# Performance work log

Measured on AMD Instinct MI355X. Metric: run time of the kernel, lower is better.

## Reference

```python
import jax, jax.numpy as jnp
import numpy as np
from functools import lru_cache

B_IN, B_L1, B_L2 = 112, 28, 14


def _wigner_ds(l, betas):
    """Wigner-d matrices d^l_{m'm}(beta) (quantum norm, centered order, CS phase)
    via d(beta) = expm(beta*K), K = -(J+ - J-)/2 real antisymmetric; iK is
    Hermitian so we eigendecompose once and phase-rotate for all betas."""
    if l == 0:
        return np.ones((len(betas), 1, 1))
    m = np.arange(-l, l)
    c = np.sqrt(l * (l + 1) - m * (m + 1))  # ladder coefficients m -> m+1
    K = np.zeros((2 * l + 1, 2 * l + 1))
    i = np.arange(2 * l)
    K[i + 1, i] = -0.5 * c
    K[i, i + 1] = 0.5 * c
    lam, V = np.linalg.eigh(1j * K)
    ph = np.exp(-1j * np.outer(betas, lam))  # [n_beta, 2l+1]
    return np.einsum('ak,bk,ck->bac', V, ph, V.conj()).real  # [n_beta, m', m]


def _quad_weights(b):
    """Kostelec-Rockmore SOFT quadrature weights on the 2b beta grid."""
    j = np.arange(2 * b)
    k = np.arange(b)
    s = (np.sin(np.pi * (2 * j[:, None] + 1) * (2 * k[None, :] + 1) / (4. * b))
         / (2 * k[None, :] + 1)).sum(1)
    w = (2. / b) * np.sin(np.pi * (2 * j + 1) / (4. * b)) * s
    return (w * 2. * np.pi / (2 * b) ** 2).astype(np.float32)


@lru_cache(maxsize=None)
def _s2_wigner(b, nl):
    """Weighted forward-S2-FFT table: n=0 column of d^l, [2b, nl^2]."""
    betas = (np.arange(2 * b) + 0.5) / (2 * b) * np.pi
    w = _quad_weights(b)
    cols = [_wigner_ds(l, betas)[:, :, l] * w[:, None] for l in range(nl)]
    return np.concatenate(cols, 1).astype(np.float32)


@lru_cache(maxsize=None)
def _so3_wigner(b, nl, weighted):
    """SO3 transform table: [2b, sum_l (2l+1)^2]; quadrature-weighted for the
    forward transform, (2l+1)-scaled for the inverse."""
    betas = (np.arange(2 * b) + 0.5) / (2 * b) * np.pi
    w = _quad_weights(b)
    cols = []
    for l in range(nl):
        d = _wigner_ds(l, betas)
        d = d * (w[:, None, None] if weighted else float(2 * l + 1))
        cols.append(d.reshape(2 * b, -1))
    return np.concatenate(cols, 1).astype(np.float32)


def _freq_idx(l, n):
    # centered frequencies m=-l..l mapped to FFT bin order of an n-point FFT
    return np.concatenate([np.arange(n - l, n), np.arange(l + 1)]) if l > 0 else np.arange(1)


def s2_fft(x, b_in, b_out):
    # x: complex [z, 2b, 2b] over (beta, alpha) -> spectral [b_out^2, z]
    wig = _s2_wigner(b_in, b_out)
    xf = jnp.fft.fft(x, axis=2)  # FFT over alpha, unnormalized
    outs = []
    for l in range(b_out):
        w = jnp.asarray(wig[:, l * l:l * l + 2 * l + 1]).astype(x.dtype)
        xx = xf[:, :, _freq_idx(l, 2 * b_in)]
        outs.append(jnp.einsum('bm,zbm->mz', w, xx))
    return jnp.concatenate(outs, 0)


def so3_fft(x, b_in, b_out):
    # x: complex [z, 2b, 2b, 2b] over (beta, alpha, gamma) -> [nspec, z]
    wig = _so3_wigner(b_in, b_out, True)
    xf = jnp.fft.fftn(x, axes=(2, 3))
    outs, begin = [], 0
    for l in range(b_out):
        L = 2 * l + 1
        idx = _freq_idx(l, 2 * b_in)
        xx = xf[:, :, idx[:, None], idx[None, :]]
        w = jnp.asarray(wig[:, begin:begin + L * L].reshape(2 * b_in, L, L)).astype(x.dtype)
        outs.append(jnp.einsum('bmn,zbmn->mnz', w, xx).reshape(L * L, -1))
        begin += L * L
    return jnp.concatenate(outs, 0)


def so3_rifft(spec, b):
    # spec: complex [sum_{l<b}(2l+1)^2, z] -> real [z, 2b, 2b, 2b]
    wig = _so3_wigner(b, b, False)
    z = spec.shape[1]
    F = jnp.zeros((z, 2 * b, 2 * b, 2 * b), spec.dtype)
    begin = 0
    for l in range(b):
        L = 2 * l + 1
        sl = spec[begin:begin + L * L].reshape(L, L, z)
        w = jnp.asarray(wig[:, begin:begin + L * L].reshape(2 * b, L, L)).astype(spec.dtype)
        t = jnp.einsum('mnz,bmn->zbmn', sl, w)
        idx = _freq_idx(l, 2 * b)
        F = F.at[:, :, idx[:, None], idx[None, :]].add(t)
        begin += L * L
    # unnormalized inverse FFT over (alpha, gamma), matching torch.ifft * (2b)^2
    return (jnp.fft.ifftn(F, axes=(2, 3)) * (2 * b) ** 2).real


def s2_conv(x, w, bias, b_in, b_out):
    B, Cin = x.shape[0], x.shape[1]
    Cout = w.shape[2]
    xs = s2_fft(x.reshape(B * Cin, 2 * b_in, 2 * b_in).astype(jnp.complex64), b_in, b_out)
    xs = xs.reshape(-1, B, Cin)  # [l*m, B, Cin]
    y = jax.lax.complex(w[..., 0], w[..., 1])  # [l*m, Cin, Cout]
    outs = []
    for l in range(b_out):  # s2_mm: z_l[m,n] = sum_i x_l[m,i] conj(y_l[n,i])
        s = slice(l * l, l * l + 2 * l + 1)
        Fz = jnp.einsum('mzi,nio->mnzo', xs[s], jnp.conj(y[s]))
        outs.append(Fz.reshape(-1, B, Cout))
    zs = jnp.concatenate(outs, 0).reshape(-1, B * Cout)
    out = so3_rifft(zs, b_out).reshape(B, Cout, 2 * b_out, 2 * b_out, 2 * b_out)
    return out + bias


def so3_conv(x, w, bias, b_in, b_out):
    B, Cin = x.shape[0], x.shape[1]
    Cout = w.shape[2]
    xs = so3_fft(x.reshape(B * Cin, 2 * b_in, 2 * b_in, 2 * b_in).astype(jnp.complex64), b_in, b_out)
    xs = xs.reshape(-1, B, Cin)  # [l*m*n, B, Cin]
    y = jax.lax.complex(w[..., 0], w[..., 1])  # [l*m*n, Cin, Cout]
    outs, begin = [], 0
    for l in range(b_out):  # so3_mm: z_l[m,n] = sum_{k,i} conj(x_l[m,k,i]) y_l[n,k,i]
        L = 2 * l + 1
        X = xs[begin:begin + L * L].reshape(L, L, B, Cin)
        Y = y[begin:begin + L * L].reshape(L, L, Cin, Cout)
        Fz = jnp.einsum('mkzi,nkio->mnzo', jnp.conj(X), Y)
        outs.append(Fz.reshape(L * L, B, Cout))
        begin += L * L
    zs = jnp.concatenate(outs, 0).reshape(-1, B * Cout)
    out = so3_rifft(zs, b_out).reshape(B, Cout, 2 * b_out, 2 * b_out, 2 * b_out)
    return out + bias


def so3_integrate(x):
    # x: [B, C, beta, alpha, gamma]; sum over alpha,gamma + quadrature over beta
    b = x.shape[-1] // 2
    w = jnp.asarray(_quad_weights(b))
    return jnp.einsum('zcbag,b->zc', x, w)


def _nspec_so3(b):
    return b * (4 * b * b - 1) // 3


def setup_inputs() -> dict:
    key = jax.random.key(0)
    ks = jax.random.split(key, 8)
    B = 4
    sc = 1e-3  # keep activations in a sane range through 5 spectral convs
    return {
        'x': jax.random.normal(ks[0], (B, 3, 2 * B_IN, 2 * B_IN), jnp.float32),
        'w1': jax.random.normal(ks[1], (B_L1 ** 2, 3, 32, 2), jnp.float32) * sc,
        'b1': jnp.zeros((1, 32, 1, 1, 1), jnp.float32),
        'w2': jax.random.normal(ks[2], (_nspec_so3(B_L2), 32, 64, 2), jnp.float32) * sc,
        'b2': jnp.zeros((1, 64, 1, 1, 1), jnp.float32),
        'w3': jax.random.normal(ks[3], (_nspec_so3(B_L2), 64, 128, 2), jnp.float32) * sc,
        'b3': jnp.zeros((1, 128, 1, 1, 1), jnp.float32),
        'w4': jax.random.normal(ks[4], (_nspec_so3(B_L2), 128, 64, 2), jnp.float32) * sc,
        'b4': jnp.zeros((1, 64, 1, 1, 1), jnp.float32),
        'w5': jax.random.normal(ks[5], (_nspec_so3(B_L2), 64, 40, 2), jnp.float32) * sc,
        'b5': jnp.zeros((1, 40, 1, 1, 1), jnp.float32),
        'w_out': jax.random.normal(ks[6], (10, 40), jnp.float32) * 0.1,
        'b_out': jnp.zeros((10,), jnp.float32),
    }


def reference(x, w1, b1, w2, b2, w3, b3, w4, b4, w5, b5, w_out, b_out):
    h = jax.nn.relu(s2_conv(x, w1, b1, B_IN, B_L1))
    h = jax.nn.relu(so3_conv(h, w2, b2, B_L1, B_L2))
    h = jax.nn.relu(so3_conv(h, w3, b3, B_L2, B_L2))
    h = jax.nn.relu(so3_conv(h, w4, b4, B_L2, B_L2))
    h = jax.nn.relu(so3_conv(h, w5, b5, B_L2, B_L2))
    h = so3_integrate(h)
    return h @ w_out.T + b_out
```

## Files before the change

### kernel.cpp

```cpp
#include <hip/hip_runtime.h>
#include <cmath>
#include <cstring>
#include <vector>



__global__ void kg_idx(int4* __restrict__ LMN28, int4* __restrict__ LMN14,
                       int* __restrict__ IDX1) {
  int l = blockIdx.x;
  int L = 2*l + 1, ofs = l*(4*l*l - 1)/3;
  for (int i = threadIdx.x; i < L*L; i += blockDim.x) {
    int a = i / L, c = i - a*L;
    int4 v = make_int4(l, a - l, c - l, 0);
    LMN28[ofs + i] = v;
    if (l < 14) LMN14[ofs + i] = v;
  }
  for (int a = threadIdx.x; a < L; a += blockDim.x)
    IDX1[l*l + a] = (a - l) + 27;
}

__global__ void kg_tw(float2* __restrict__ E224, float2* __restrict__ EF56,
                      float2* __restrict__ EI56, float2* __restrict__ EF28,
                      float2* __restrict__ EI28) {
  int t = blockIdx.x*256 + threadIdx.x;
  const float TP = 6.283185307179586f;
  if (t < 12320) {
    int mi = t/224, a = t - mi*224;
    int r = ((mi - 27)*a) % 224;
    float ang = -TP*r/224.f;
    E224[t] = make_float2(cosf(ang), sinf(ang)); return;
  }
  t -= 12320;
  if (t < 1512) {
    int ki = t/56, g = t - ki*56;
    int r = ((ki - 13)*g) % 56;
    float ang = -TP*r/56.f;
    EF56[t] = make_float2(cosf(ang), sinf(ang)); return;
  }
  t -= 1512;
  if (t < 3080) {
    int a = t/55, mi = t - a*55;
    int r = ((mi - 27)*a) % 56;
    float ang = TP*r/56.f;
    EI56[t] = make_float2(cosf(ang), sinf(ang)); return;
  }
  t -= 3080;
  if (t < 756) {
    int ki = t/28, g = t - ki*28;
    int r = ((ki - 13)*g) % 28;
    float ang = -TP*r/28.f;
    EF28[t] = make_float2(cosf(ang), sinf(ang)); return;
  }
  t -= 756;
  if (t < 756) {
    int a = t/27, mi = t - a*27;
    int r = ((mi - 13)*a) % 28;
    float ang = TP*r/28.f;
// ... 228 lines not shown
  }
}

template<int NA, int NF>
__global__ __launch_bounds__(256)
void kf2_dfta(const float2* __restrict__ XA, const float2* __restrict__ EF,
              float2* __restrict__ Xf, int rowsC) {
  int ki = blockIdx.x;
  int mt = blockIdx.y;
  int row = blockIdx.z*256 + threadIdx.x;
  if (row >= rowsC) return;
  float2 acc[14];
  #pragma unroll
  for (int u = 0; u < 14; ++u) acc[u] = make_float2(0.f, 0.f);
  const float2* xp = XA + (size_t)ki*rowsC + row;
  for (int a = 0; a < NA; ++a) {
    float2 v = xp[(size_t)a*NF*rowsC];
    #pragma unroll
    for (int u = 0; u < 14; ++u) {
      int mi = mt*14 + u; if (mi >= NF) mi = NF-1;
      float2 e = EF[mi*NA + a];
      acc[u].x += v.x*e.x - v.y*e.y;
      acc[u].y += v.x*e.y + v.y*e.x;
    }
  }
  #pragma unroll
  for (int u = 0; u < 14; ++u) {
    int mi = mt*14 + u;
    if (mi < NF) Xf[((size_t)mi*NF + ki)*rowsC + row] = acc[u];
  }
}

__global__ void k8_wigfwd(const float2* __restrict__ XfT,
                          const float* __restrict__ WT,
                          const int4* __restrict__ LMN,
                          float2* __restrict__ XS,
                          int NB, int ZC, int z0, int Ztot) {
  int spec = blockIdx.x;
  int zl = threadIdx.x;
  int4 t = LMN[spec];
  int mi = t.y + 13, ni = t.z + 13;
  float2 acc = make_float2(0.f, 0.f);
  size_t base = (size_t)(mi*27 + ni) * ((size_t)NB*ZC);
  for (int b = 0; b < NB; ++b) {
    float w = WT[(size_t)spec*NB + b];
    float2 v = XfT[base + (size_t)b*ZC + zl];
    acc.x += w*v.x; acc.y += w*v.y;
  }
  XS[(size_t)spec*Ztot + z0 + zl] = acc;
}

template<int CI, int CO>
__global__ __launch_bounds__(256)
void k9_gemm3(const float2* __restrict__ XS, const float2* __restrict__ W,
              const int4* __restrict__ tasks, float2* __restrict__ ZSo) {
  constexpr int Zin = 4*CI, Zout = 4*CO;
  constexpr int LOG2CI = (CI==32) ? 5 : (CI==64) ? 6 : 7;
  int4 tk = tasks[blockIdx.x];
  int l = tk.x, m0 = tk.y, c0 = tk.z;
  int L = 2*l + 1;
  int ofs = l*(4*l*l - 1)/3;
  int N = L*CO, K = L*CI;
  __shared__ float2 As[16][33];
  __shared__ float2 Bs[16][64];
  int t = threadIdx.x;
  int ob = t & 63, kb0 = t >> 6;
  int c = c0 + ob;
  bool colOK = c < N;
  int n = colOK ? c / CO : 0;
  int o = c - n*CO;
  size_t bbase = ((size_t)(ofs + n*L))*(size_t)(CI*CO) + o;
  int q = t >> 6, j = t & 63;
  float2 acc[8];
  #pragma unroll
  for (int u = 0; u < 8; ++u) acc[u] = make_float2(0.f, 0.f);

  for (int k0 = 0; k0 < K; k0 += 16) {
    #pragma unroll
    for (int h = 0; h < 2; ++h) {
      int fi = t + h*256;
      int row = fi >> 4, tc = fi & 15;
      int m = m0 + (row >> 2), zb = row & 3;
      int kk = k0 + tc;
      float2 av = make_float2(0.f, 0.f);
      if (m < L) {
        int kq = kk >> LOG2CI, ii = kk & (CI-1);
        float2 xv = XS[((size_t)(ofs + m*L + kq))*Zin + (size_t)zb*CI + ii];
        av = make_float2(xv.x, -xv.y);
      }
      As[tc][row] = av;
    }
    #pragma unroll
    for (int j2 = 0; j2 < 4; ++j2) {
      int kb = kb0*4 + j2;
      float2 wv = make_float2(0.f, 0.f);
      if (colOK) wv = W[bbase + (size_t)(k0 + kb)*CO];
      Bs[kb][ob] = wv;
    }
    __syncthreads();
    for (int kk2 = 0; kk2 < 16; ++kk2) {
      float2 b = Bs[kk2][j];
      #pragma unroll
      for (int u = 0; u < 8; ++u) {
        float2 a = As[kk2][u*4 + q];
        acc[u].x += a.x*b.x - a.y*b.y;
        acc[u].y += a.x*b.y + a.y*b.x;
      }
    }
    __syncthreads();
  }
  if (colOK) {
    #pragma unroll
    for (int u = 0; u < 8; ++u) {
      int m = m0 + u;
      if (m < L) {
        ZSo[((size_t)(ofs + m*L + n))*Zout + (size_t)q*CO + o] = acc[u];
      }
    }
  }
}

__global__ void k10a_colsum(const float* __restrict__ Ht, float* __restrict__ Cp,
                            int rows, int cols, int rowsPer) {
  int col = blockIdx.x*256 + threadIdx.x;
  if (col >= cols) return;
  int r0 = blockIdx.y*rowsPer;
  int r1 = r0 + rowsPer; if (r1 > rows) r1 = rows;
  float acc = 0.f;
  for (int r = r0; r < r1; ++r) acc += Ht[(size_t)r*cols + col];
  Cp[(size_t)blockIdx.y*cols + col] = acc;
}

__global__ void k10a_fin(const float* __restrict__ Cp, const float* __restrict__ QW,
                         float* __restrict__ S, int Zt, int NB, int nparts) {
  int z = blockIdx.x*64 + threadIdx.x;
  if (z >= Zt) return;
  int cols = NB*Zt;
  float acc = 0.f;
  for (int b = 0; b < NB; ++b) {
    float cs = 0.f;
    for (int p = 0; p < nparts; ++p) cs += Cp[(size_t)p*cols + b*Zt + z];
    acc += cs * QW[b];
  }
  S[z] = acc;
}

__global__ void k10b_fc(const float* __restrict__ S,
                        const float* __restrict__ Wout,
                        const float* __restrict__ bout,
                        float* __restrict__ out) {
  int t = threadIdx.x;
  if (t < 40) {
    int zb = t / 10, c = t % 10;
    float acc = bout[c];
    for (int o = 0; o < 40; ++o) acc += S[zb*40 + o] * Wout[c*40 + o];
    out[zb*10 + c] = acc;
  }
}


static const size_t U_VT    = 0;
static const size_t U_LAM   = 117040;
static const size_t U_QW224 = U_LAM + 3136;
static const size_t U_QW56  = U_QW224 + 896;
static const size_t U_QW28  = U_QW56 + 224;
static const size_t U_TK2   = U_QW28 + 112;
static const size_t U_TK3   = U_TK2 + 24576;
static const size_t U_TK4   = U_TK3 + 24576;
static const size_t U_TK5   = U_TK4 + 24576;
static const size_t U_BYTES = U_TK5 + 24576;

struct WsOff {
  size_t up, ws2t, wi28t, wf28t, wi14t, wf14t, e224, ef56, ei56, ef28, ei28,
         lmn28, lmn14, idx1, zs1, xsf, zso, HA, HB, S, fixedEnd;
};

static WsOff wsOff() {
  WsOff o; size_t c = 0;
  auto take = [&](size_t bytes) { size_t r = c; c = (c + bytes + 255) & ~(size_t)255; return r; };
  o.up    = take(U_BYTES);
  o.ws2t  = take((size_t)784*224*4);
  o.wi28t = take((size_t)29260*56*4);
  o.wf28t = take((size_t)3654*56*4);
  o.wi14t = take((size_t)3654*28*4);
  o.wf14t = take((size_t)3654*28*4);
  o.e224  = take((size_t)55*224*8);
  o.ef56  = take((size_t)27*56*8);
  o.ei56  = take((size_t)56*55*8);
  o.ef28  = take((size_t)27*28*8);
  o.ei28  = take((size_t)28*27*8);
  o.lmn28 = take((size_t)29260*16);
  o.lmn14 = take((size_t)3654*16);
  o.idx1  = take(784*4);
  o.zs1   = take((size_t)29260*128*8);
  o.xsf   = take((size_t)3654*512*8);
  o.zso   = take((size_t)3654*512*8);
  o.HA    = take((size_t)128*56*56*56*4);
  o.HB    = take((size_t)512*28*28*28*4);
  o.S     = take(16*4480*4 + 1024);
  o.fixedEnd = c;
  return o;
}

static void jacobi_sym(int n, double* A, double* V, double* lam) {
  for (int i = 0; i < n*n; ++i) V[i] = 0.0;
  for (int i = 0; i < n; ++i) V[i*n + i] = 1.0;
  for (int sweep = 0; sweep < 100; ++sweep) {
    double off = 0.0;
    for (int p = 0; p < n; ++p)
      for (int q = p+1; q < n; ++q) off += A[p*n+q]*A[p*n+q];
    if (off < 1e-22) break;
    for (int p = 0; p < n-1; ++p) {
      for (int q = p+1; q < n; ++q) {
        double apq = A[p*n+q];
        if (fabs(apq) < 1e-300) continue;
        double theta = (A[q*n+q] - A[p*n+p]) / (2.0*apq);
        double tt = (theta >= 0 ? 1.0 : -1.0) / (fabs(theta) + sqrt(theta*theta + 1.0));
        double cc = 1.0/sqrt(tt*tt + 1.0), ss = tt*cc;
        for (int i = 0; i < n; ++i) {
          double aip = A[i*n+p], aiq = A[i*n+q];
          A[i*n+p] = cc*aip - ss*aiq;
          A[i*n+q] = ss*aip + cc*aiq;
        }
        for (int i = 0; i < n; ++i) {
          double api = A[p*n+i], aqi = A[q*n+i];
          A[p*n+i] = cc*api - ss*aqi;
          A[q*n+i] = ss*api + cc*aqi;
        }
        for (int i = 0; i < n; ++i) {
          double vip = V[i*n+p], viq = V[i*n+q];
          V[i*n+p] = cc*vip - ss*viq;
          V[i*n+q] = ss*vip + cc*viq;
        }
      }
    }
  }
  for (int i = 0; i < n; ++i) lam[i] = A[i*n+i];
}

extern "C" void kernel_launch(void* const* d_in, const int* in_sizes, int n_in,
                              void* d_out, int out_size, void* d_ws, size_t ws_size,
                              hipStream_t stream) {
  (void)in_sizes; (void)n_in; (void)out_size;
  const WsOff off = wsOff();
  const size_t MINAB = (size_t)3080*32*56*8;
  if (ws_size < off.fixedEnd + 2*MINAB) return;

  const float*  x    = (const float*)d_in[0];
  const float2* w1   = (const float2*)d_in[1];
  const float*  b1   = (const float*)d_in[2];
  const float2* w2   = (const float2*)d_in[3];
  const float*  b2   = (const float*)d_in[4];
  const float2* w3   = (const float2*)d_in[5];
  const float*  b3   = (const float*)d_in[6];
  const float2* w4   = (const float2*)d_in[7];
  const float*  b4   = (const float*)d_in[8];
  const float2* w5   = (const float2*)d_in[9];
  const float*  b5   = (const float*)d_in[10];
  const float*  wout = (const float*)d_in[11];
  const float*  bout = (const float*)d_in[12];
  float* outp = (float*)d_out;
  char* ws = (char*)d_ws;

  char* hb = new char[U_BYTES];
  memset(hb, 0, U_BYTES);
  float* hVT  = (float*)(hb + U_VT);
  float* hLAM = (float*)(hb + U_LAM);
  float* hQW224 = (float*)(hb + U_QW224);
  float* hQW56  = (float*)(hb + U_QW56);
  float* hQW28  = (float*)(hb + U_QW28);
  int4*  hTK[4] = {(int4*)(hb + U_TK2), (int4*)(hb + U_TK3),
                   (int4*)(hb + U_TK4), (int4*)(hb + U_TK5)};

  auto quadw = [](int b, double* w) {
    for (int j = 0; j < 2*b; ++j) {
      double s = 0.0;
      for (int k = 0; k < b; ++k)
        s += sin(M_PI*(2*j+1)*(2*k+1)/(4.0*b)) / (double)(2*k+1);
      w[j] = 2.0/b * sin(M_PI*(2*j+1)/(4.0*b)) * s * 2.0*M_PI/((2.0*b)*(2.0*b));
    }
  };
  std::vector<double> qw224(224), qw56(56), qw28v(28);
  quadw(112, qw224.data()); quadw(28, qw56.data()); quadw(14, qw28v.data());
  for (int j = 0; j < 224; ++j) hQW224[j] = (float)qw224[j];
  for (int j = 0; j < 56;  ++j) hQW56[j]  = (float)qw56[j];
  for (int j = 0; j < 28;  ++j) hQW28[j]  = (float)qw28v[j];

  const int NMAX = 55;
  std::vector<double> T(NMAX*NMAX), V(NMAX*NMAX), lam(NMAX);
  for (int l = 0; l < 28; ++l) {
    int n = 2*l + 1;
    std::fill(T.begin(), T.begin() + n*n, 0.0);
    for (int i = 0; i < n-1; ++i) {
      int m = i - l;
      double c = sqrt((double)(l*(l+1)) - (double)(m*(m+1)));
      T[i*n + i + 1] = 0.5*c;
      T[(i+1)*n + i] = 0.5*c;
    }
    jacobi_sym(n, T.data(), V.data(), lam.data());
    size_t vofs = (size_t)l*(4*l*l - 1)/3;
    for (int i = 0; i < n*n; ++i) hVT[vofs + i] = (float)V[i];
    for (int k = 0; k < n; ++k)  hLAM[l*l + k] = (float)lam[k];
  }

  const int COv[4] = {64, 128, 64, 40};
  int tcnt[4];
  for (int li = 0; li < 4; ++li) {
    int cnt = 0;
    for (int l = 13; l >= 0; --l) {
      int L = 2*l + 1, N = L*COv[li];
      for (int c0 = 0; c0 < N; c0 += 64)
        for (int m0 = 0; m0 < L; m0 += 8)
          hTK[li][cnt++] = make_int4(l, m0, c0, 0);
    }
    tcnt[li] = cnt;
  }

  const float*  dWS2T  = (const float*)(ws + off.ws2t);
  const float*  dWI28T = (const float*)(ws + off.wi28t);
  const float*  dWF28T = (const float*)(ws + off.wf28t);
  const float*  dWI14T = (const float*)(ws + off.wi14t);
  const float*  dWF14T = (const float*)(ws + off.wf14t);
  const float2* dE224  = (const float2*)(ws + off.e224);
  const float2* dEF56  = (const float2*)(ws + off.ef56);
  const float2* dEI56  = (const float2*)(ws + off.ei56);
  const float2* dEF28  = (const float2*)(ws + off.ef28);
  const float2* dEI28  = (const float2*)(ws + off.ei28);
  const int4*   dLMN28 = (const int4*)(ws + off.lmn28);
  const int4*   dLMN14 = (const int4*)(ws + off.lmn14);
  const int*    dIDX1  = (const int*)(ws + off.idx1);
  const float*  dUVT   = (const float*)(ws + off.up + U_VT);
  const float*  dULAM  = (const float*)(ws + off.up + U_LAM);
  const float*  dUQW224= (const float*)(ws + off.up + U_QW224);
  const float*  dUQW56 = (const float*)(ws + off.up + U_QW56);
  const float*  dUQW28 = (const float*)(ws + off.up + U_QW28);
  const int4*   dTK2   = (const int4*)(ws + off.up + U_TK2);
  const int4*   dTK3   = (const int4*)(ws + off.up + U_TK3);
  const int4*   dTK4   = (const int4*)(ws + off.up + U_TK4);
  const int4*   dTK5   = (const int4*)(ws + off.up + U_TK5);
  float2* dZS1 = (float2*)(ws + off.zs1);
  float2* dXSF = (float2*)(ws + off.xsf);
  float2* dZSO = (float2*)(ws + off.zso);
  float*  dHA  = (float*)(ws + off.HA);
  float*  dHB  = (float*)(ws + off.HB);
  float*  dCp  = (float*)(ws + off.S);
  float*  dS   = (float*)(ws + off.S + 16*4480*4);

  size_t ab = ((ws_size - off.fixedEnd)/2) & ~(size_t)255;
  char* Abuf = ws + off.fixedEnd;
  char* Bbuf = Abuf + ab;
  float2* dA = (float2*)Abuf;
  float2* dB = (float2*)Bbuf;
  float2* dXF1 = (float2*)Abuf;
  float2* dXS1 = (float2*)(Abuf + 1182720);

  hipMemcpyAsync(ws + off.up, hb, U_BYTES, hipMemcpyHostToDevice, stream);
  kg_idx<<<28, 256, 0, stream>>>((int4*)(ws + off.lmn28), (int4*)(ws + off.lmn14),
                                 (int*)(ws + off.idx1));
  kg_tw<<<72, 256, 0, stream>>>((float2*)(ws + off.e224), (float2*)(ws + off.ef56),
                                (float2*)(ws + off.ei56), (float2*)(ws + off.ef28),
                                (float2*)(ws + off.ei28));
  kg_wig<<<784, 224, 0, stream>>>(dUVT, dULAM, dUQW224, nullptr,
                                  (float*)(ws + off.ws2t), 224, 0);
  kg_wig<<<29260, 64, 0, stream>>>(dUVT, dULAM, nullptr, dLMN28,
                                   (float*)(ws + off.wi28t), 56, 1);
  kg_wig<<<3654, 64, 0, stream>>>(dUVT, dULAM, dUQW56, dLMN14,
                                  (float*)(ws + off.wf28t), 56, 2);
  kg_wig<<<3654, 64, 0, stream>>>(dUVT, dULAM, nullptr, dLMN14,
                                  (float*)(ws + off.wi14t), 28, 1);
  kg_wig<<<3654, 64, 0, stream>>>(dUVT, dULAM, dUQW28, dLMN14,
                                  (float*)(ws + off.wf14t), 28, 2);

  auto pickPow2 = [&](int Zt, size_t perz)->int {
    int zc = Zt;
    while (zc > 32 && perz*(size_t)zc > ab) zc >>= 1;
    return zc;
  };
  int zc1  = pickPow2(128, (size_t)3080*56*8);
  int zcF2 = pickPow2(128, (size_t)56*27*56*8);
  int zcI  = pickPow2(256, (size_t)756*28*8);
  int zcF  = pickPow2(256, (size_t)28*27*28*8);

  k1_dft_alpha<<<12*224, 64, 0, stream>>>(x, dE224, dXF1);
  k2_s2wig<<<784, 64, 0, stream>>>(dXF1, dWS2T, dIDX1, dXS1);
  k3_combine1<<<29260, 128, 0, stream>>>(dXS1, w1, dLMN28, dZS1);
  for (int z0 = 0; z0 < 128; z0 += zc1) {
    int rowsC = zc1*56;
    k4_wiginv<56,28><<<dim3(3025, zc1/32), 256, 0, stream>>>(dZS1, dWI28T, dA, 128, z0, zc1);
    k5a_idft<55,56><<<dim3(55, 7, (rowsC+255)/256), 256, 0, stream>>>(dA, dEI56, dB, rowsC);
    k5b_idft<55,56><<<dim3(56, (rowsC+63)/64), 256, 0, stream>>>(dB, dEI56, b1, dHA,
                                                                 zc1, z0, 128, 56, 32, rowsC);
  }

  for (int z0 = 0; z0 < 128; z0 += zcF2) {
    int rowsC = zcF2*56;
    kf1_dftg<56,27><<<dim3(56, 2, (rowsC+255)/256), 256, 0, stream>>>(dHA, dEF56, dA,
                                                                      56, 128, z0, zcF2, rowsC);
    kf2_dfta<56,27><<<dim3(27, 2, (rowsC+255)/256), 256, 0, stream>>>(dA, dEF56, dB, rowsC);
    k8_wigfwd<<<3654, zcF2, 0, stream>>>(dB, dWF28T, dLMN14, dXSF, 56, zcF2, z0, 128);
  }
  k9_gemm3<32,64><<<tcnt[0], 256, 0, stream>>>(dXSF, w2, dTK2, dZSO);
  for (int z0 = 0; z0 < 256; z0 += zcI) {
    int rowsC = zcI*28;
    k4_wiginv<28,14><<<dim3(729, zcI/32), 256, 0, stream>>>(dZSO, dWI14T, dA, 256, z0, zcI);
    k5a_idft<27,28><<<dim3(27, 4, (rowsC+255)/256), 256, 0, stream>>>(dA, dEI28, dB, rowsC);
    k5b_idft<27,28><<<dim3(28, (rowsC+63)/64), 256, 0, stream>>>(dB, dEI28, b2, dHB,
                                                                 zcI, z0, 256, 28, 64, rowsC);
  }

  for (int z0 = 0; z0 < 256; z0 += zcF) {
    int rowsC = zcF*28;
    kf1_dftg<28,27><<<dim3(28, 2, (rowsC+255)/256), 256, 0, stream>>>(dHB, dEF28, dA,
                                                                      28, 256, z0, zcF, rowsC);
    kf2_dfta<28,27><<<dim3(27, 2, (rowsC+255)/256), 256, 0, stream>>>(dA, dEF28, dB, rowsC);
    k8_wigfwd<<<3654, zcF, 0, stream>>>(dB, dWF14T, dLMN14, dXSF, 28, zcF, z0, 256);
  }
  k9_gemm3<64,128><<<tcnt[1], 256, 0, stream>>>(dXSF, w3, dTK3, dZSO);
  for (int z0 = 0; z0 < 512; z0 += zcI) {
    int rowsC = zcI*28;
    k4_wiginv<28,14><<<dim3(729, zcI/32), 256, 0, stream>>>(dZSO, dWI14T, dA, 512, z0, zcI);
    k5a_idft<27,28><<<dim3(27, 4, (rowsC+255)/256), 256, 0, stream>>>(dA, dEI28, dB, rowsC);
    k5b_idft<27,28><<<dim3(28, (rowsC+63)/64), 256, 0, stream>>>(dB, dEI28, b3, dHA,
                                                                 zcI, z0, 512, 28, 128, rowsC);
  }

  for (int z0 = 0; z0 < 512; z0 += zcF) {
    int rowsC = zcF*28;
    kf1_dftg<28,27><<<dim3(28, 2, (rowsC+255)/256), 256, 0, stream>>>(dHA, dEF28, dA,
                                                                      28, 512, z0, zcF, rowsC);
    kf2_dfta<28,27><<<dim3(27, 2, (rowsC+255)/256), 256, 0, stream>>>(dA, dEF28, dB, rowsC);
    k8_wigfwd<<<3654, zcF, 0, stream>>>(dB, dWF14T, dLMN14, dXSF, 28, zcF, z0, 512);
  }
  k9_gemm3<128,64><<<tcnt[2], 256, 0, stream>>>(dXSF, w4, dTK4, dZSO);
  for (int z0 = 0; z0 < 256; z0 += zcI) {
    int rowsC = zcI*28;
    k4_wiginv<28,14><<<dim3(729, zcI/32), 256, 0, stream>>>(dZSO, dWI14T, dA, 256, z0, zcI);
    k5a_idft<27,28><<<dim3(27, 4, (rowsC+255)/256), 256, 0, stream>>>(dA, dEI28, dB, rowsC);
    k5b_idft<27,28><<<dim3(28, (rowsC+63)/64), 256, 0, stream>>>(dB, dEI28, b4, dHB,
                                                                 zcI, z0, 256, 28, 64, rowsC);
  }

  for (int z0 = 0; z0 < 256; z0 += zcF) {
    int rowsC = zcF*28;
    kf1_dftg<28,27><<<dim3(28, 2, (rowsC+255)/256), 256, 0, stream>>>(dHB, dEF28, dA,
                                                                      28, 256, z0, zcF, rowsC);
    kf2_dfta<28,27><<<dim3(27, 2, (rowsC+255)/256), 256, 0, stream>>>(dA, dEF28, dB, rowsC);
    k8_wigfwd<<<3654, zcF, 0, stream>>>(dB, dWF14T, dLMN14, dXSF, 28, zcF, z0, 256);
  }
  k9_gemm3<64,40><<<tcnt[3], 256, 0, stream>>>(dXSF, w5, dTK5, dZSO);
  {
    int rowsC = 160*28;
    k4_wiginv<28,14><<<dim3(729, 5), 256, 0, stream>>>(dZSO, dWI14T, dA, 160, 0, 160);
    k5a_idft<27,28><<<dim3(27, 4, (rowsC+255)/256), 256, 0, stream>>>(dA, dEI28, dB, rowsC);
    k5b_idft<27,28><<<dim3(28, (rowsC+63)/64), 256, 0, stream>>>(dB, dEI28, b5, dHA,
                                                                 160, 0, 160, 28, 40, rowsC);
  }

  k10a_colsum<<<dim3(18, 16), 256, 0, stream>>>(dHA, dCp, 784, 4480, 49);
  k10a_fin<<<3, 64, 0, stream>>>(dCp, dUQW28, dS, 160, 28, 16);
  k10b_fc<<<1, 64, 0, stream>>>(dS, wout, bout, outp);
}
```

Measured before the change: 4.336 ms.

## Retile spectral GEMM so each block covers all m rows with register prefetch

The per-degree complex GEMM is reorganised so each block owns 32 output columns (n,o) and the full 4L set of (m,z) rows, instead of 8 m-rows by 64 columns. This means each weight element is read from global memory once rather than once per m-tile. Next-step weight and input tiles are loaded into registers while the current tile is computed from shared memory. The cost is 14 accumulators per thread with predicated work that is wasted for small l, and fewer blocks in flight.

```diff
diff --git a/kernel.cpp b/kernel.cpp
--- a/kernel.cpp
+++ b/kernel.cpp
@@ -337,69 +337,104 @@
 
 template<int CI, int CO>
 __global__ __launch_bounds__(256)
-void k9_gemm3(const float2* __restrict__ XS, const float2* __restrict__ W,
-              const int4* __restrict__ tasks, float2* __restrict__ ZSo) {
+void k9_gemm5(const float2* __restrict__ XS, const float2* __restrict__ W,
+              const int2* __restrict__ tasks, float2* __restrict__ ZSo) {
   constexpr int Zin = 4*CI, Zout = 4*CO;
   constexpr int LOG2CI = (CI==32) ? 5 : (CI==64) ? 6 : 7;
-  int4 tk = tasks[blockIdx.x];
-  int l = tk.x, m0 = tk.y, c0 = tk.z;
+  int2 tk = tasks[blockIdx.x];
+  int l = tk.x, no0 = tk.y;
   int L = 2*l + 1;
   int ofs = l*(4*l*l - 1)/3;
+  int C = 4*L;
   int N = L*CO, K = L*CI;
-  __shared__ float2 As[16][33];
-  __shared__ float2 Bs[16][64];
+  __shared__ float2 Ws[16][32];
+  __shared__ float2 Xs[16][129];
   int t = threadIdx.x;
-  int ob = t & 63, kb0 = t >> 6;
-  int c = c0 + ob;
-  bool colOK = c < N;
-  int n = colOK ? c / CO : 0;
-  int o = c - n*CO;
-  size_t bbase = ((size_t)(ofs + n*L))*(size_t)(CI*CO) + o;
-  int q = t >> 6, j = t & 63;
-  float2 acc[8];
-  #pragma unroll
-  for (int u = 0; u < 8; ++u) acc[u] = make_float2(0.f, 0.f);
-
-  for (int k0 = 0; k0 < K; k0 += 16) {
-    #pragma unroll
-    for (int h = 0; h < 2; ++h) {
-      int fi = t + h*256;
-      int row = fi >> 4, tc = fi & 15;
-      int m = m0 + (row >> 2), zb = row & 3;
-      int kk = k0 + tc;
-      float2 av = make_float2(0.f, 0.f);
-      if (m < L) {
-        int kq = kk >> LOG2CI, ii = kk & (CI-1);
-        float2 xv = XS[((size_t)(ofs + m*L + kq))*Zin + (size_t)zb*CI + ii];
-        av = make_float2(xv.x, -xv.y);
+  int row = t & 31, cg = t >> 5;
+  int nrow = no0 + row;
+  bool rowOK = nrow < N;
+  int n = rowOK ? nrow / CO : 0;
+  int o = nrow - n*CO;
+  size_t wbase = ((size_t)(ofs + n*L))*(size_t)(CI*CO) + o;
+
+  float2 acc[14];
+  #pragma unroll
+  for (int u = 0; u < 14; ++u) acc[u] = make_float2(0.f, 0.f);
+  float2 wreg[2];
+  float2 xreg[7];
+  int nsteps = K >> 4;
+
+  #pragma unroll
+  for (int h = 0; h < 2; ++h) {
+    int kk = cg + h*8;
+    wreg[h] = rowOK ? W[wbase + (size_t)kk*CO] : make_float2(0.f, 0.f);
+  }
+  #pragma unroll
+  for (int h = 0; h < 7; ++h) {
+    int f = t + h*256;
+    int kk = f & 15, col = f >> 4;
+    float2 v = make_float2(0.f, 0.f);
+    if (col < C) {
+      int kq = kk >> LOG2CI, ii = kk & (CI-1);
+      int m = col >> 2, zb = col & 3;
+      float2 xv = XS[((size_t)(ofs + m*L + kq))*Zin + (size_t)zb*CI + ii];
+      v = make_float2(xv.x, -xv.y);
+    }
+    xreg[h] = v;
+  }
+
+  for (int ks = 0; ks < nsteps; ++ks) {
+    __syncthreads();
+    #pragma unroll
+    for (int h = 0; h < 2; ++h) Ws[cg + h*8][row] = wreg[h];
+    #pragma unroll
+    for (int h = 0; h < 7; ++h) {
+      int f = t + h*256;
+      if ((f >> 4) < 128) Xs[f & 15][f >> 4] = xreg[h];
+    }
+    __syncthreads();
+    if (ks + 1 < nsteps) {
+      int k0 = (ks + 1)*16;
+      #pragma unroll
+      for (int h = 0; h < 2; ++h) {
+        int kk = k0 + cg + h*8;
+        wreg[h] = rowOK ? W[wbase + (size_t)kk*CO] : make_float2(0.f, 0.f);
       }
-      As[tc][row] = av;
-    }
-    #pragma unroll
-    for (int j2 = 0; j2 < 4; ++j2) {
-      int kb = kb0*4 + j2;
-      float2 wv = make_float2(0.f, 0.f);
-      if (colOK) wv = W[bbase + (size_t)(k0 + kb)*CO];
-      Bs[kb][ob] = wv;
-    }
-    __syncthreads();
-    for (int kk2 = 0; kk2 < 16; ++kk2) {
-      float2 b = Bs[kk2][j];
       #pragma unroll
-      for (int u = 0; u < 8; ++u) {
-        float2 a = As[kk2][u*4 + q];
-        acc[u].x += a.x*b.x - a.y*b.y;
-        acc[u].y += a.x*b.y + a.y*b.x;
+      for (int h = 0; h < 7; ++h) {
+        int f = t + h*256;
+        int kk = k0 + (f & 15), col = f >> 4;
+        float2 v = make_float2(0.f, 0.f);
+        if (col < C) {
+          int kq = kk >> LOG2CI, ii = kk & (CI-1);
+          int m = col >> 2, zb = col & 3;
+          float2 xv = XS[((size_t)(ofs + m*L + kq))*Zin + (size_t)zb*CI + ii];
+          v = make_float2(xv.x, -xv.y);
+        }
+        xreg[h] = v;
       }
     }
-    __syncthreads();
-  }
-  if (colOK) {
-    #pragma unroll
-    for (int u = 0; u < 8; ++u) {
-      int m = m0 + u;
-      if (m < L) {
-        ZSo[((size_t)(ofs + m*L + n))*Zout + (size_t)q*CO + o] = acc[u];
+    #pragma unroll
+    for (int kk = 0; kk < 16; ++kk) {
+      float2 w = Ws[kk][row];
+      #pragma unroll
+      for (int u = 0; u < 14; ++u) {
+        int col = cg + u*8;
+        if (col < C) {
+          float2 xv = Xs[kk][col];
+          acc[u].x += xv.x*w.x - xv.y*w.y;
+          acc[u].y += xv.x*w.y + xv.y*w.x;
+        }
+      }
+    }
+  }
+  if (rowOK) {
+    #pragma unroll
+    for (int u = 0; u < 14; ++u) {
+      int col = cg + u*8;
+      if (col < C) {
+        int m = col >> 2, zb = col & 3;
+        ZSo[((size_t)(ofs + m*L + n))*Zout + (size_t)zb*CO + o] = acc[u];
       }
     }
   }
@@ -554,8 +589,8 @@
   float* hQW224 = (float*)(hb + U_QW224);
   float* hQW56  = (float*)(hb + U_QW56);
   float* hQW28  = (float*)(hb + U_QW28);
-  int4*  hTK[4] = {(int4*)(hb + U_TK2), (int4*)(hb + U_TK3),
-                   (int4*)(hb + U_TK4), (int4*)(hb + U_TK5)};
+  int2*  hTK[4] = {(int2*)(hb + U_TK2), (int2*)(hb + U_TK3),
+                   (int2*)(hb + U_TK4), (int2*)(hb + U_TK5)};
 
   auto quadw = [](int b, double* w) {
     for (int j = 0; j < 2*b; ++j) {
@@ -594,9 +629,8 @@
     int cnt = 0;
     for (int l = 13; l >= 0; --l) {
       int L = 2*l + 1, N = L*COv[li];
-      for (int c0 = 0; c0 < N; c0 += 64)
-        for (int m0 = 0; m0 < L; m0 += 8)
-          hTK[li][cnt++] = make_int4(l, m0, c0, 0);
+      for (int no0 = 0; no0 < N; no0 += 32)
+        hTK[li][cnt++] = make_int2(l, no0);
     }
     tcnt[li] = cnt;
   }
@@ -619,10 +653,10 @@
   const float*  dUQW224= (const float*)(ws + off.up + U_QW224);
   const float*  dUQW56 = (const float*)(ws + off.up + U_QW56);
   const float*  dUQW28 = (const float*)(ws + off.up + U_QW28);
-  const int4*   dTK2   = (const int4*)(ws + off.up + U_TK2);
-  const int4*   dTK3   = (const int4*)(ws + off.up + U_TK3);
-  const int4*   dTK4   = (const int4*)(ws + off.up + U_TK4);
-  const int4*   dTK5   = (const int4*)(ws + off.up + U_TK5);
+  const int2*   dTK2   = (const int2*)(ws + off.up + U_TK2);
+  const int2*   dTK3   = (const int2*)(ws + off.up + U_TK3);
+  const int2*   dTK4   = (const int2*)(ws + off.up + U_TK4);
+  const int2*   dTK5   = (const int2*)(ws + off.up + U_TK5);
   float2* dZS1 = (float2*)(ws + off.zs1);
   float2* dXSF = (float2*)(ws + off.xsf);
   float2* dZSO = (float2*)(ws + off.zso);
@@ -684,7 +718,7 @@
     kf2_dfta<56,27><<<dim3(27, 2, (rowsC+255)/256), 256, 0, stream>>>(dA, dEF56, dB, rowsC);
     k8_wigfwd<<<3654, zcF2, 0, stream>>>(dB, dWF28T, dLMN14, dXSF, 56, zcF2, z0, 128);
   }
-  k9_gemm3<32,64><<<tcnt[0], 256, 0, stream>>>(dXSF, w2, dTK2, dZSO);
+  k9_gemm5<32,64><<<tcnt[0], 256, 0, stream>>>(dXSF, w2, dTK2, dZSO);
   for (int z0 = 0; z0 < 256; z0 += zcI) {
     int rowsC = zcI*28;
     k4_wiginv<28,14><<<dim3(729, zcI/32), 256, 0, stream>>>(dZSO, dWI14T, dA, 256, z0, zcI);
@@ -700,7 +734,7 @@
     kf2_dfta<28,27><<<dim3(27, 2, (rowsC+255)/256), 256, 0, stream>>>(dA, dEF28, dB, rowsC);
     k8_wigfwd<<<3654, zcF, 0, stream>>>(dB, dWF14T, dLMN14, dXSF, 28, zcF, z0, 256);
   }
-  k9_gemm3<64,128><<<tcnt[1], 256, 0, stream>>>(dXSF, w3, dTK3, dZSO);
+  k9_gemm5<64,128><<<tcnt[1], 256, 0, stream>>>(dXSF, w3, dTK3, dZSO);
   for (int z0 = 0; z0 < 512; z0 += zcI) {
     int rowsC = zcI*28;
     k4_wiginv<28,14><<<dim3(729, zcI/32), 256, 0, stream>>>(dZSO, dWI14T, dA, 512, z0, zcI);
@@ -716,7 +750,7 @@
     kf2_dfta<28,27><<<dim3(27, 2, (rowsC+255)/256), 256, 0, stream>>>(dA, dEF28, dB, rowsC);
     k8_wigfwd<<<3654, zcF, 0, stream>>>(dB, dWF14T, dLMN14, dXSF, 28, zcF, z0, 512);
   }
-  k9_gemm3<128,64><<<tcnt[2], 256, 0, stream>>>(dXSF, w4, dTK4, dZSO);
+  k9_gemm5<128,64><<<tcnt[2], 256, 0, stream>>>(dXSF, w4, dTK4, dZSO);
   for (int z0 = 0; z0 < 256; z0 += zcI) {
     int rowsC = zcI*28;
     k4_wiginv<28,14><<<dim3(729, zcI/32), 256, 0, stream>>>(dZSO, dWI14T, dA, 256, z0, zcI);
@@ -732,7 +766,7 @@
     kf2_dfta<28,27><<<dim3(27, 2, (rowsC+255)/256), 256, 0, stream>>>(dA, dEF28, dB, rowsC);
     k8_wigfwd<<<3654, zcF, 0, stream>>>(dB, dWF14T, dLMN14, dXSF, 28, zcF, z0, 256);
   }
-  k9_gemm3<64,40><<<tcnt[3], 256, 0, stream>>>(dXSF, w5, dTK5, dZSO);
+  k9_gemm5<64,40><<<tcnt[3], 256, 0, stream>>>(dXSF, w5, dTK5, dZSO);
   {
     int rowsC = 160*28;
     k4_wiginv<28,14><<<dim3(729, 5), 256, 0, stream>>>(dZSO, dWI14T, dA, 160, 0, 160);
```

After: 7.859 ms. 81.2% more time.

## Split-K the per-degree spectral GEMM for high l and reduce partials

Applied to the files above, without the earlier changes.

For degrees l>=8, the spectral GEMM's K dimension is split into NS chunks so that more blocks run in parallel on the long, tail-heavy high-l tasks. Partial results from the extra chunks go to a scratch buffer, and a new add kernel folds them into the output. This trades extra global writes, reads and a launch for better load balance and occupancy. It also reuses the B buffer as partial storage and grows the task tables.

```diff
diff --git a/kernel.cpp b/kernel.cpp
--- a/kernel.cpp
+++ b/kernel.cpp
@@ -337,15 +337,23 @@
 
 template<int CI, int CO>
 __global__ __launch_bounds__(256)
-void k9_gemm3(const float2* __restrict__ XS, const float2* __restrict__ W,
-              const int4* __restrict__ tasks, float2* __restrict__ ZSo) {
+void k9_gemm7(const float2* __restrict__ XS, const float2* __restrict__ W,
+              const int4* __restrict__ tasks, float2* __restrict__ ZSo,
+              float2* __restrict__ P, size_t pstride, int NS, int L0) {
   constexpr int Zin = 4*CI, Zout = 4*CO;
   constexpr int LOG2CI = (CI==32) ? 5 : (CI==64) ? 6 : 7;
   int4 tk = tasks[blockIdx.x];
-  int l = tk.x, m0 = tk.y, c0 = tk.z;
+  int l = tk.x, m0 = tk.y, c0 = tk.z, ks = tk.w;
   int L = 2*l + 1;
   int ofs = l*(4*l*l - 1)/3;
   int N = L*CO, K = L*CI;
+  int kb = 0, ke = K;
+  float2* out = ZSo;
+  if (l >= L0) {
+    int chunk = (K/16/NS)*16;
+    kb = ks*chunk; ke = kb + chunk;
+    if (ks > 0) out = P + (size_t)(ks - 1)*pstride;
+  }
   __shared__ float2 As[16][33];
   __shared__ float2 Bs[16][64];
   int t = threadIdx.x;
@@ -360,7 +368,7 @@
   #pragma unroll
   for (int u = 0; u < 8; ++u) acc[u] = make_float2(0.f, 0.f);
 
-  for (int k0 = 0; k0 < K; k0 += 16) {
+  for (int k0 = kb; k0 < ke; k0 += 16) {
     #pragma unroll
     for (int h = 0; h < 2; ++h) {
       int fi = t + h*256;
@@ -377,10 +385,10 @@
     }
     #pragma unroll
     for (int j2 = 0; j2 < 4; ++j2) {
-      int kb = kb0*4 + j2;
+      int kb2 = kb0*4 + j2;
       float2 wv = make_float2(0.f, 0.f);
-      if (colOK) wv = W[bbase + (size_t)(k0 + kb)*CO];
-      Bs[kb][ob] = wv;
+      if (colOK) wv = W[bbase + (size_t)(k0 + kb2)*CO];
+      Bs[kb2][ob] = wv;
     }
     __syncthreads();
     for (int kk2 = 0; kk2 < 16; ++kk2) {
@@ -399,10 +407,22 @@
     for (int u = 0; u < 8; ++u) {
       int m = m0 + u;
       if (m < L) {
-        ZSo[((size_t)(ofs + m*L + n))*Zout + (size_t)q*CO + o] = acc[u];
+        out[((size_t)(ofs + m*L + n))*Zout + (size_t)q*CO + o] = acc[u];
       }
     }
   }
+}
+
+__global__ void kadd(float2* __restrict__ Z, const float2* __restrict__ P,
+                     size_t pstride, size_t offset, size_t count, int nparts) {
+  size_t i = (size_t)blockIdx.x*256 + threadIdx.x;
+  if (i >= count) return;
+  float2 v = Z[offset + i];
+  for (int p = 0; p < nparts; ++p) {
+    float2 w = P[(size_t)p*pstride + offset + i];
+    v.x += w.x; v.y += w.y;
+  }
+  Z[offset + i] = v;
 }
 
 __global__ void k10a_colsum(const float* __restrict__ Ht, float* __restrict__ Cp,
@@ -450,10 +470,10 @@
 static const size_t U_QW56  = U_QW224 + 896;
 static const size_t U_QW28  = U_QW56 + 224;
 static const size_t U_TK2   = U_QW28 + 112;
-static const size_t U_TK3   = U_TK2 + 24576;
-static const size_t U_TK4   = U_TK3 + 24576;
-static const size_t U_TK5   = U_TK4 + 24576;
-static const size_t U_BYTES = U_TK5 + 24576;
+static const size_t U_TK3   = U_TK2 + 32768;
+static const size_t U_TK4   = U_TK3 + 32768;
+static const size_t U_TK5   = U_TK4 + 32768;
+static const size_t U_BYTES = U_TK5 + 32768;
 
 struct WsOff {
   size_t up, ws2t, wi28t, wf28t, wi14t, wf14t, e224, ef56, ei56, ef28, ei28,
@@ -589,14 +609,18 @@
   }
 
   const int COv[4] = {64, 128, 64, 40};
+  const int NSv[4] = {2, 2, 4, 2};
+  const int L0 = 8;
   int tcnt[4];
   for (int li = 0; li < 4; ++li) {
     int cnt = 0;
     for (int l = 13; l >= 0; --l) {
       int L = 2*l + 1, N = L*COv[li];
+      int ns = (l >= L0) ? NSv[li] : 1;
       for (int c0 = 0; c0 < N; c0 += 64)
         for (int m0 = 0; m0 < L; m0 += 8)
-          hTK[li][cnt++] = make_int4(l, m0, c0, 0);
+          for (int ks = 0; ks < ns; ++ks)
+            hTK[li][cnt++] = make_int4(l, m0, c0, ks);
     }
     tcnt[li] = cnt;
   }
@@ -636,6 +660,7 @@
   char* Bbuf = Abuf + ab;
   float2* dA = (float2*)Abuf;
   float2* dB = (float2*)Bbuf;
+  float2* dPart = (float2*)Bbuf;
   float2* dXF1 = (float2*)Abuf;
   float2* dXS1 = (float2*)(Abuf + 1182720);
 
@@ -666,6 +691,14 @@
   int zcI  = pickPow2(256, (size_t)756*28*8);
   int zcF  = pickPow2(256, (size_t)28*27*28*8);
 
+  auto launch_kadd = [&](int Zout, int nparts) {
+    size_t pstride = (size_t)3654*Zout;
+    size_t offs = (size_t)680*Zout;
+    size_t count = (size_t)(3654 - 680)*Zout;
+    kadd<<<(int)((count + 255)/256), 256, 0, stream>>>(dZSO, dPart, pstride,
+                                                       offs, count, nparts);
+  };
+
   k1_dft_alpha<<<12*224, 64, 0, stream>>>(x, dE224, dXF1);
   k2_s2wig<<<784, 64, 0, stream>>>(dXF1, dWS2T, dIDX1, dXS1);
   k3_combine1<<<29260, 128, 0, stream>>>(dXS1, w1, dLMN28, dZS1);
@@ -684,7 +717,9 @@
     kf2_dfta<56,27><<<dim3(27, 2, (rowsC+255)/256), 256, 0, stream>>>(dA, dEF56, dB, rowsC);
     k8_wigfwd<<<3654, zcF2, 0, stream>>>(dB, dWF28T, dLMN14, dXSF, 56, zcF2, z0, 128);
   }
-  k9_gemm3<32,64><<<tcnt[0], 256, 0, stream>>>(dXSF, w2, dTK2, dZSO);
+  k9_gemm7<32,64><<<tcnt[0], 256, 0, stream>>>(dXSF, w2, dTK2, dZSO,
+                                               dPart, (size_t)3654*256, 2, L0);
+  launch_kadd(256, 1);
   for (int z0 = 0; z0 < 256; z0 += zcI) {
     int rowsC = zcI*28;
     k4_wiginv<28,14><<<dim3(729, zcI/32), 256, 0, stream>>>(dZSO, dWI14T, dA, 256, z0, zcI);
@@ -700,7 +735,9 @@
     kf2_dfta<28,27><<<dim3(27, 2, (rowsC+255)/256), 256, 0, stream>>>(dA, dEF28, dB, rowsC);
     k8_wigfwd<<<3654, zcF, 0, stream>>>(dB, dWF14T, dLMN14, dXSF, 28, zcF, z0, 256);
   }
-  k9_gemm3<64,128><<<tcnt[1], 256, 0, stream>>>(dXSF, w3, dTK3, dZSO);
+  k9_gemm7<64,128><<<tcnt[1], 256, 0, stream>>>(dXSF, w3, dTK3, dZSO,
+                                                dPart, (size_t)3654*512, 2, L0);
+  launch_kadd(512, 1);
   for (int z0 = 0; z0 < 512; z0 += zcI) {
     int rowsC = zcI*28;
     k4_wiginv<28,14><<<dim3(729, zcI/32), 256, 0, stream>>>(dZSO, dWI14T, dA, 512, z0, zcI);
@@ -716,7 +753,9 @@
     kf2_dfta<28,27><<<dim3(27, 2, (rowsC+255)/256), 256, 0, stream>>>(dA, dEF28, dB, rowsC);
     k8_wigfwd<<<3654, zcF, 0, stream>>>(dB, dWF14T, dLMN14, dXSF, 28, zcF, z0, 512);
   }
-  k9_gemm3<128,64><<<tcnt[2], 256, 0, stream>>>(dXSF, w4, dTK4, dZSO);
+  k9_gemm7<128,64><<<tcnt[2], 256, 0, stream>>>(dXSF, w4, dTK4, dZSO,
+                                                dPart, (size_t)3654*256, 4, L0);
+  launch_kadd(256, 3);
   for (int z0 = 0; z0 < 256; z0 += zcI) {
     int rowsC = zcI*28;
     k4_wiginv<28,14><<<dim3(729, zcI/32), 256, 0, stream>>>(dZSO, dWI14T, dA, 256, z0, zcI);
@@ -732,7 +771,9 @@
     kf2_dfta<28,27><<<dim3(27, 2, (rowsC+255)/256), 256, 0, stream>>>(dA, dEF28, dB, rowsC);
     k8_wigfwd<<<3654, zcF, 0, stream>>>(dB, dWF14T, dLMN14, dXSF, 28, zcF, z0, 256);
   }
-  k9_gemm3<64,40><<<tcnt[3], 256, 0, stream>>>(dXSF, w5, dTK5, dZSO);
+  k9_gemm7<64,40><<<tcnt[3], 256, 0, stream>>>(dXSF, w5, dTK5, dZSO,
+                                               dPart, (size_t)3654*160, 2, L0);
+  launch_kadd(160, 1);
   {
     int rowsC = 160*28;
     k4_wiginv<28,14><<<dim3(729, 5), 256, 0, stream>>>(dZSO, dWI14T, dA, 160, 0, 160);
```

Result: slower. 4.631 ms (+6.8%).

## Run SO3 spectral complex GEMMs on bf16 MFMA with split-precision emulation

Applied to the files above, without the earlier changes.

Replaces the scalar FP32 complex GEMM in the SO3 convolution layers with an MFMA 16x16x32 bf16 kernel. Each complex operand is split into hi and lo bf16 parts, and three MFMAs (hh, hl, lh) approximate FP32 accuracy. Complex multiplication is encoded as a real GEMM by interleaving real and imaginary parts, with a sign-flipped B layout. Tasks are repacked into single ints. The goal is higher matrix throughput, at the cost of conversion work, smaller tiles with a sync per 16-complex k-step, and slightly lower precision.

```diff
diff --git a/kernel.cpp b/kernel.cpp
--- a/kernel.cpp
+++ b/kernel.cpp
@@ -3,6 +3,16 @@
 #include <cstring>
 #include <vector>
 
+
+using sv8 = __attribute__((ext_vector_type(8))) short;
+using fv4 = __attribute__((ext_vector_type(4))) float;
+
+__device__ __forceinline__ unsigned short bhi(float v) {
+  return (unsigned short)(__float_as_uint(v) >> 16);
+}
+__device__ __forceinline__ float bf2f(unsigned short h) {
+  return __uint_as_float(((unsigned)h) << 16);
+}
 
 
 __global__ void kg_idx(int4* __restrict__ LMN28, int4* __restrict__ LMN14,
@@ -337,69 +347,86 @@
 
 template<int CI, int CO>
 __global__ __launch_bounds__(256)
-void k9_gemm3(const float2* __restrict__ XS, const float2* __restrict__ W,
-              const int4* __restrict__ tasks, float2* __restrict__ ZSo) {
+void k9_mfma(const float2* __restrict__ XS, const float2* __restrict__ W,
+             const int* __restrict__ tasks, float* __restrict__ ZSo) {
   constexpr int Zin = 4*CI, Zout = 4*CO;
   constexpr int LOG2CI = (CI==32) ? 5 : (CI==64) ? 6 : 7;
-  int4 tk = tasks[blockIdx.x];
-  int l = tk.x, m0 = tk.y, c0 = tk.z;
+  int pk = tasks[blockIdx.x];
+  int l  = pk & 15;
+  int m0 = ((pk >> 4) & 15)*16;
+  int c0 = (pk >> 8)*64;
   int L = 2*l + 1;
   int ofs = l*(4*l*l - 1)/3;
-  int N = L*CO, K = L*CI;
-  __shared__ float2 As[16][33];
-  __shared__ float2 Bs[16][64];
+  int M = 4*L, K = L*CI, N2 = 2*L*CO;
+  __shared__ __align__(16) unsigned short Ah[16][40], Al[16][40];
+  __shared__ __align__(16) unsigned short Bh[64][40], Bl[64][40];
   int t = threadIdx.x;
-  int ob = t & 63, kb0 = t >> 6;
-  int c = c0 + ob;
-  bool colOK = c < N;
-  int n = colOK ? c / CO : 0;
-  int o = c - n*CO;
-  size_t bbase = ((size_t)(ofs + n*L))*(size_t)(CI*CO) + o;
-  int q = t >> 6, j = t & 63;
-  float2 acc[8];
-  #pragma unroll
-  for (int u = 0; u < 8; ++u) acc[u] = make_float2(0.f, 0.f);
-
-  for (int k0 = 0; k0 < K; k0 += 16) {
+  int wv = t >> 6, ln = t & 63;
+  int frow = ln & 15, fkg = ln >> 4;
+  fv4 acc = {0.f, 0.f, 0.f, 0.f};
+
+  int ar = t >> 4, atc = t & 15;
+  int AR = m0 + ar;
+  int am = AR >> 2, azb = AR & 3;
+  bool aok = AR < M;
+  int nc0 = c0 >> 1;
+
+  for (int k20 = 0; k20 < 2*K; k20 += 32) {
+    int kc0 = k20 >> 1;
+    {
+      int kc = kc0 + atc;
+      float xr = 0.f, xi = 0.f;
+      if (aok) {
+        int kq = kc >> LOG2CI, ii = kc & (CI-1);
+        float2 xv = XS[((size_t)(ofs + am*L + kq))*Zin + (size_t)azb*CI + ii];
+        xr = xv.x; xi = -xv.y;
+      }
+      unsigned short rh = bhi(xr); unsigned short rl = bhi(xr - bf2f(rh));
+      unsigned short ih = bhi(xi); unsigned short il = bhi(xi - bf2f(ih));
+      *(unsigned*)&Ah[ar][2*atc] = (unsigned)rh | ((unsigned)ih << 16);
+      *(unsigned*)&Al[ar][2*atc] = (unsigned)rl | ((unsigned)il << 16);
+    }
     #pragma unroll
     for (int h = 0; h < 2; ++h) {
-      int fi = t + h*256;
-      int row = fi >> 4, tc = fi & 15;
-      int m = m0 + (row >> 2), zb = row & 3;
-      int kk = k0 + tc;
-      float2 av = make_float2(0.f, 0.f);
-      if (m < L) {
-        int kq = kk >> LOG2CI, ii = kk & (CI-1);
-        float2 xv = XS[((size_t)(ofs + m*L + kq))*Zin + (size_t)zb*CI + ii];
-        av = make_float2(xv.x, -xv.y);
+      int idx = t + 256*h;
+      int kci = idx >> 5, nci = idx & 31;
+      int kc = kc0 + kci;
+      int nc = nc0 + nci;
+      float wr = 0.f, wi = 0.f;
+      if (nc < L*CO) {
+        int n = nc / CO, o = nc - n*CO;
+        int kq = kc >> LOG2CI, ii = kc & (CI-1);
+        float2 wvv = W[((size_t)(ofs + n*L + kq)*CI + ii)*CO + o];
+        wr = wvv.x; wi = wvv.y;
       }
-      As[tc][row] = av;
-    }
+      unsigned short rh = bhi(wr); unsigned short rl = bhi(wr - bf2f(rh));
+      unsigned short ih = bhi(wi); unsigned short il = bhi(wi - bf2f(ih));
+      *(unsigned*)&Bh[2*nci][2*kci]     = (unsigned)rh | ((unsigned)(ih ^ 0x8000) << 16);
+      *(unsigned*)&Bh[2*nci + 1][2*kci] = (unsigned)ih | ((unsigned)rh << 16);
+      *(unsigned*)&Bl[2*nci][2*kci]     = (unsigned)rl | ((unsigned)(il ^ 0x8000) << 16);
+      *(unsigned*)&Bl[2*nci + 1][2*kci] = (unsigned)il | ((unsigned)rl << 16);
+    }
+    __syncthreads();
+    sv8 fah = *(const sv8*)&Ah[frow][fkg*8];
+    sv8 fal = *(const sv8*)&Al[frow][fkg*8];
+    sv8 fbh = *(const sv8*)&Bh[wv*16 + frow][fkg*8];
+    sv8 fbl = *(const sv8*)&Bl[wv*16 + frow][fkg*8];
+    acc = __builtin_amdgcn_mfma_f32_16x16x32_bf16(fah, fbh, acc, 0, 0, 0);
+    acc = __builtin_amdgcn_mfma_f32_16x16x32_bf16(fah, fbl, acc, 0, 0, 0);
+    acc = __builtin_amdgcn_mfma_f32_16x16x32_bf16(fal, fbh, acc, 0, 0, 0);
+    __syncthreads();
+  }
+  int col = ln & 15;
+  int n2 = c0 + wv*16 + col;
+  if (n2 < N2) {
+    int nc = n2 >> 1, comp = n2 & 1;
+    int n = nc / CO, o = nc - n*CO;
     #pragma unroll
-    for (int j2 = 0; j2 < 4; ++j2) {
-      int kb = kb0*4 + j2;
-      float2 wv = make_float2(0.f, 0.f);
-      if (colOK) wv = W[bbase + (size_t)(k0 + kb)*CO];
-      Bs[kb][ob] = wv;
-    }
-    __syncthreads();
-    for (int kk2 = 0; kk2 < 16; ++kk2) {
-      float2 b = Bs[kk2][j];
-      #pragma unroll
-      for (int u = 0; u < 8; ++u) {
-        float2 a = As[kk2][u*4 + q];
-        acc[u].x += a.x*b.x - a.y*b.y;
-        acc[u].y += a.x*b.y + a.y*b.x;
-      }
-    }
-    __syncthreads();
-  }
-  if (colOK) {
-    #pragma unroll
-    for (int u = 0; u < 8; ++u) {
-      int m = m0 + u;
-      if (m < L) {
-        ZSo[((size_t)(ofs + m*L + n))*Zout + (size_t)q*CO + o] = acc[u];
+    for (int g = 0; g < 4; ++g) {
+      int R = m0 + (ln >> 4)*4 + g;
+      if (R < M) {
+        int m = R >> 2, zb = R & 3;
+        ZSo[(((size_t)(ofs + m*L + n))*Zout + (size_t)zb*CO + o)*2 + comp] = acc[g];
       }
     }
   }
@@ -554,8 +581,8 @@
   float* hQW224 = (float*)(hb + U_QW224);
   float* hQW56  = (float*)(hb + U_QW56);
   float* hQW28  = (float*)(hb + U_QW28);
-  int4*  hTK[4] = {(int4*)(hb + U_TK2), (int4*)(hb + U_TK3),
-                   (int4*)(hb + U_TK4), (int4*)(hb + U_TK5)};
+  int*   hTK[4] = {(int*)(hb + U_TK2), (int*)(hb + U_TK3),
+                   (int*)(hb + U_TK4), (int*)(hb + U_TK5)};
 
   auto quadw = [](int b, double* w) {
     for (int j = 0; j < 2*b; ++j) {
@@ -593,10 +620,10 @@
   for (int li = 0; li < 4; ++li) {
     int cnt = 0;
     for (int l = 13; l >= 0; --l) {
-      int L = 2*l + 1, N = L*COv[li];
-      for (int c0 = 0; c0 < N; c0 += 64)
-        for (int m0 = 0; m0 < L; m0 += 8)
-          hTK[li][cnt++] = make_int4(l, m0, c0, 0);
+      int L = 2*l + 1, M = 4*L, N2 = 2*L*COv[li];
+      for (int c0 = 0; c0 < N2; c0 += 64)
+        for (int m0 = 0; m0 < M; m0 += 16)
+          hTK[li][cnt++] = l | ((m0/16) << 4) | ((c0/64) << 8);
     }
     tcnt[li] = cnt;
   }
@@ -619,10 +646,10 @@
   const float*  dUQW224= (const float*)(ws + off.up + U_QW224);
   const float*  dUQW56 = (const float*)(ws + off.up + U_QW56);
   const float*  dUQW28 = (const float*)(ws + off.up + U_QW28);
-  const int4*   dTK2   = (const int4*)(ws + off.up + U_TK2);
-  const int4*   dTK3   = (const int4*)(ws + off.up + U_TK3);
-  const int4*   dTK4   = (const int4*)(ws + off.up + U_TK4);
-  const int4*   dTK5   = (const int4*)(ws + off.up + U_TK5);
+  const int*    dTK2   = (const int*)(ws + off.up + U_TK2);
+  const int*    dTK3   = (const int*)(ws + off.up + U_TK3);
+  const int*    dTK4   = (const int*)(ws + off.up + U_TK4);
+  const int*    dTK5   = (const int*)(ws + off.up + U_TK5);
   float2* dZS1 = (float2*)(ws + off.zs1);
   float2* dXSF = (float2*)(ws + off.xsf);
   float2* dZSO = (float2*)(ws + off.zso);
@@ -684,7 +711,7 @@
     kf2_dfta<56,27><<<dim3(27, 2, (rowsC+255)/256), 256, 0, stream>>>(dA, dEF56, dB, rowsC);
     k8_wigfwd<<<3654, zcF2, 0, stream>>>(dB, dWF28T, dLMN14, dXSF, 56, zcF2, z0, 128);
   }
-  k9_gemm3<32,64><<<tcnt[0], 256, 0, stream>>>(dXSF, w2, dTK2, dZSO);
+  k9_mfma<32,64><<<tcnt[0], 256, 0, stream>>>(dXSF, w2, dTK2, (float*)dZSO);
   for (int z0 = 0; z0 < 256; z0 += zcI) {
     int rowsC = zcI*28;
     k4_wiginv<28,14><<<dim3(729, zcI/32), 256, 0, stream>>>(dZSO, dWI14T, dA, 256, z0, zcI);
@@ -700,7 +727,7 @@
     kf2_dfta<28,27><<<dim3(27, 2, (rowsC+255)/256), 256, 0, stream>>>(dA, dEF28, dB, rowsC);
     k8_wigfwd<<<3654, zcF, 0, stream>>>(dB, dWF14T, dLMN14, dXSF, 28, zcF, z0, 256);
   }
-  k9_gemm3<64,128><<<tcnt[1], 256, 0, stream>>>(dXSF, w3, dTK3, dZSO);
+  k9_mfma<64,128><<<tcnt[1], 256, 0, stream>>>(dXSF, w3, dTK3, (float*)dZSO);
   for (int z0 = 0; z0 < 512; z0 += zcI) {
     int rowsC = zcI*28;
     k4_wiginv<28,14><<<dim3(729, zcI/32), 256, 0, stream>>>(dZSO, dWI14T, dA, 512, z0, zcI);
@@ -716,7 +743,7 @@
     kf2_dfta<28,27><<<dim3(27, 2, (rowsC+255)/256), 256, 0, stream>>>(dA, dEF28, dB, rowsC);
     k8_wigfwd<<<3654, zcF, 0, stream>>>(dB, dWF14T, dLMN14, dXSF, 28, zcF, z0, 512);
   }
-  k9_gemm3<128,64><<<tcnt[2], 256, 0, stream>>>(dXSF, w4, dTK4, dZSO);
+  k9_mfma<128,64><<<tcnt[2], 256, 0, stream>>>(dXSF, w4, dTK4, (float*)dZSO);
   for (int z0 = 0; z0 < 256; z0 += zcI) {
     int rowsC = zcI*28;
     k4_wiginv<28,14><<<dim3(729, zcI/32), 256, 0, stream>>>(dZSO, dWI14T, dA, 256, z0, zcI);
@@ -732,7 +759,7 @@
     kf2_dfta<28,27><<<dim3(27, 2, (rowsC+255)/256), 256, 0, stream>>>(dA, dEF28, dB, rowsC);
     k8_wigfwd<<<3654, zcF, 0, stream>>>(dB, dWF14T, dLMN14, dXSF, 28, zcF, z0, 256);
   }
-  k9_gemm3<64,40><<<tcnt[3], 256, 0, stream>>>(dXSF, w5, dTK5, dZSO);
+  k9_mfma<64,40><<<tcnt[3], 256, 0, stream>>>(dXSF, w5, dTK5, (float*)dZSO);
   {
     int rowsC = 160*28;
     k4_wiginv<28,14><<<dim3(729, 5), 256, 0, stream>>>(dZSO, dWI14T, dA, 160, 0, 160);
```

After: 10.60 ms. 2.45x slower.
